# Kernel tuning notes

Hardware: AMD Instinct MI355X
Metric: run time of the kernel (lower is better)

Reference implementation:

```python
import jax, jax.numpy as jnp
import numpy as np

DIM = 256
HEADS = 8
K_RATIO = 0.25


def setup_inputs() -> dict:
    key = jax.random.key(0)
    ks = jax.random.split(key, 5)
    B, C, S = 4, DIM, 2048
    x = jax.random.normal(ks[0], (B, C, S), dtype=jnp.float32)
    # Conv1d(dim, 3*dim, 1, bias=False) weight -> (3*dim, dim)
    W_qkv = jax.random.normal(ks[1], (3 * DIM, DIM), dtype=jnp.float32) * (1.0 / np.sqrt(DIM))
    # depthwise Conv1d(3*dim, 3*dim, 3, groups=3*dim) weight -> (3*dim, 1, 3)
    W_dw = jax.random.normal(ks[2], (3 * DIM, 1, 3), dtype=jnp.float32) * (1.0 / np.sqrt(3))
    # Conv1d(dim, dim, 1, bias=False) weight -> (dim, dim)
    W_proj = jax.random.normal(ks[3], (DIM, DIM), dtype=jnp.float32) * (1.0 / np.sqrt(DIM))
    temperature = jnp.ones((HEADS, 1, 1), dtype=jnp.float32)
    return {"x": x, "W_qkv": W_qkv, "W_dw": W_dw, "W_proj": W_proj,
            "temperature": temperature}


def _l2norm(t, eps=1e-12):
    # F.normalize: x / max(||x||_2, eps)
    n = jnp.sqrt(jnp.sum(t * t, axis=-1, keepdims=True))
    return t / jnp.maximum(n, eps)


def reference(x, W_qkv, W_dw, W_proj, temperature):
    B, C, S = x.shape
    H = temperature.shape[0]
    hd = C // H
    # 1x1 conv == channel matmul
    qkv = jnp.einsum('oc,bcs->bos', W_qkv, x)  # [B, 3C, S]
    # depthwise conv, kernel 3, pad 1
    qkv = jax.lax.conv_general_dilated(
        qkv, W_dw, window_strides=(1,), padding=[(1, 1)],
        dimension_numbers=('NCH', 'OIH', 'NCH'),
        feature_group_count=3 * C)
    q, k, v = jnp.split(qkv, 3, axis=1)  # each [B, C, S]

    def to_heads(t):
        return t.reshape(B, H, hd, S).transpose(0, 1, 3, 2)  # [B, H, S, hd]

    q = _l2norm(to_heads(q))
    k = _l2norm(to_heads(k))
    v = to_heads(v)

    scores = jnp.einsum('bhsc,bhtc->bhst', q, k) * temperature  # [B,H,S,S]

    topk = max(1, min(S, int(np.ceil(K_RATIO * S))))
    vals, idx = jax.lax.top_k(scores, topk)  # [B,H,S,topk]

    # scatter top-k values into a -inf tensor along the last axis
    N = B * H * S
    sparse = jnp.full((N, S), -jnp.inf, dtype=scores.dtype)
    rows = jnp.arange(N)[:, None]
    sparse = sparse.at[rows, idx.reshape(N, topk)].set(vals.reshape(N, topk))
    sparse = jnp.clip(sparse.reshape(B, H, S, S), -10000.0, 10000.0)

    attn = jax.nn.softmax(sparse, axis=-1)  # dropout p=0.0 -> identity
    out = jnp.einsum('bhst,bhtc->bhsc', attn, v)  # [B,H,S,hd]
    out = out.transpose(0, 1, 3, 2).reshape(B, C, S)  # b (head c) s
    return jnp.einsum('oc,bcs->bos', W_proj, out)
```

## Files before the change

### kernel.cpp

```cpp
#include <hip/hip_runtime.h>
#include <math.h>

typedef __attribute__((ext_vector_type(8))) short short8;
typedef __attribute__((ext_vector_type(4))) float f32x4;
typedef __attribute__((ext_vector_type(2))) float f32x2;
typedef __attribute__((ext_vector_type(2))) unsigned int uint2v;

#define DEV __device__ __forceinline__

static constexpr int B_ = 4, C_ = 256, S_ = 2048, H_ = 8, O3_ = 768;
static constexpr int TOPK = 512;
static constexpr int QT = 16;
static constexpr int QCOLS = 512;
static constexpr int QSTR = 516;
static constexpr int QBUF = 16 * QSTR;
static constexpr int PSTH = 1024;
static constexpr int P1OFF = 2 * QBUF;
static constexpr size_t K3_LDS_BYTES = (size_t)2 * QBUF * 4;

DEV unsigned cvt_pk_bf16(float a, float b) {
  unsigned r;
  asm("v_cvt_pk_bf16_f32 %0, %1, %2" : "=v"(r) : "v"(a), "v"(b));
  return r;
}
DEV unsigned short f2bf1(float f) { return (unsigned short)(cvt_pk_bf16(f, f) & 0xFFFFu); }
DEV float bf2f(unsigned short h) { return __uint_as_float(((unsigned)h) << 16); }
DEV void hilo(float f, unsigned short& h, unsigned short& l) {
  unsigned p = cvt_pk_bf16(f, f);
  h = (unsigned short)p;
  float r = f - __uint_as_float(p << 16);
  l = (unsigned short)(cvt_pk_bf16(r, r) & 0xFFFFu);
}

__global__ void k_convw(const float* __restrict__ wqkv, const float* __restrict__ wproj,
                        unsigned short* __restrict__ wq_hi, unsigned short* __restrict__ wq_lo,
                        unsigned short* __restrict__ wproj_bf) {
  int i = blockIdx.x * 256 + threadIdx.x;
  if (i < O3_ * C_) {
    unsigned short h, l;
    hilo(wqkv[i], h, l);
    wq_hi[i] = h;
    wq_lo[i] = l;
  }
  if (i < C_ * C_) wproj_bf[i] = f2bf1(wproj[i]);
}

__global__ void k_xt(const float* __restrict__ x, unsigned short* __restrict__ xT_hi,
                     unsigned short* __restrict__ xT_lo) {
  __shared__ float t[32][33];
  int b = blockIdx.z;
  int c0 = blockIdx.y * 32, s0 = blockIdx.x * 32;
  int tx = threadIdx.x, ty = threadIdx.y;
  const float* xb = x + (size_t)b * C_ * S_;
#pragma unroll
  for (int j = 0; j < 4; ++j)
    t[ty + 8 * j][tx] = xb[(size_t)(c0 + ty + 8 * j) * S_ + s0 + tx];
  __syncthreads();
  unsigned short* hb = xT_hi + (size_t)b * S_ * C_;
  unsigned short* lb = xT_lo + (size_t)b * S_ * C_;
#pragma unroll
  for (int j = 0; j < 4; ++j) {
    unsigned short h, l;
    hilo(t[tx][ty + 8 * j], h, l);
    size_t o = (size_t)(s0 + ty + 8 * j) * C_ + c0 + tx;
    hb[o] = h;
    lb[o] = l;
  }
}

__global__ __launch_bounds__(256) void k_qkv(const unsigned short* __restrict__ w_hi,
                                             const unsigned short* __restrict__ w_lo,
                                             const unsigned short* __restrict__ x_hi,
                                             const unsigned short* __restrict__ x_lo,
                                             float* __restrict__ raw) {
  int b = blockIdx.z;
  int m0 = blockIdx.y * 64, n0 = blockIdx.x * 64;
  int tid = threadIdx.x, lane = tid & 63, wid = tid >> 6;
  int l15 = lane & 15, lh = lane >> 4;
  int wm = (wid >> 1) * 32, wn = (wid & 1) * 32;
  const unsigned short* xhb = x_hi + (size_t)b * S_ * C_;
  const unsigned short* xlb = x_lo + (size_t)b * S_ * C_;
  f32x4 acc[2][2] = {};
  int mA = m0 + wm + l15;
  int nB = n0 + wn + l15;
  for (int k0 = 0; k0 < C_; k0 += 32) {
    int kk = k0 + lh * 8;
    short8 a0h = *(const short8*)(w_hi + (size_t)mA * C_ + kk);
    short8 a1h = *(const short8*)(w_hi + (size_t)(mA + 16) * C_ + kk);
    short8 a0l = *(const short8*)(w_lo + (size_t)mA * C_ + kk);
    short8 a1l = *(const short8*)(w_lo + (size_t)(mA + 16) * C_ + kk);
    short8 b0h = *(const short8*)(xhb + (size_t)nB * C_ + kk);
    short8 b1h = *(const short8*)(xhb + (size_t)(nB + 16) * C_ + kk);
    short8 b0l = *(const short8*)(xlb + (size_t)nB * C_ + kk);
    short8 b1l = *(const short8*)(xlb + (size_t)(nB + 16) * C_ + kk);
    acc[0][0] = __builtin_amdgcn_mfma_f32_16x16x32_bf16(a0h, b0h, acc[0][0], 0, 0, 0);
    acc[0][1] = __builtin_amdgcn_mfma_f32_16x16x32_bf16(a0h, b1h, acc[0][1], 0, 0, 0);
    acc[1][0] = __builtin_amdgcn_mfma_f32_16x16x32_bf16(a1h, b0h, acc[1][0], 0, 0, 0);
    acc[1][1] = __builtin_amdgcn_mfma_f32_16x16x32_bf16(a1h, b1h, acc[1][1], 0, 0, 0);
    acc[0][0] = __builtin_amdgcn_mfma_f32_16x16x32_bf16(a0h, b0l, acc[0][0], 0, 0, 0);
    acc[0][1] = __builtin_amdgcn_mfma_f32_16x16x32_bf16(a0h, b1l, acc[0][1], 0, 0, 0);
    acc[1][0] = __builtin_amdgcn_mfma_f32_16x16x32_bf16(a1h, b0l, acc[1][0], 0, 0, 0);
    acc[1][1] = __builtin_amdgcn_mfma_f32_16x16x32_bf16(a1h, b1l, acc[1][1], 0, 0, 0);
    acc[0][0] = __builtin_amdgcn_mfma_f32_16x16x32_bf16(a0l, b0h, acc[0][0], 0, 0, 0);
    acc[0][1] = __builtin_amdgcn_mfma_f32_16x16x32_bf16(a0l, b1h, acc[0][1], 0, 0, 0);
    acc[1][0] = __builtin_amdgcn_mfma_f32_16x16x32_bf16(a1l, b0h, acc[1][0], 0, 0, 0);
    acc[1][1] = __builtin_amdgcn_mfma_f32_16x16x32_bf16(a1l, b1h, acc[1][1], 0, 0, 0);
  }
  float* rawb = raw + (size_t)b * O3_ * S_;
#pragma unroll
  for (int i = 0; i < 2; ++i)
#pragma unroll
    for (int j = 0; j < 2; ++j)
#pragma unroll
      for (int r = 0; r < 4; ++r) {
        int row = m0 + wm + i * 16 + lh * 4 + r;
        int col = n0 + wn + j * 16 + l15;
        rawb[(size_t)row * S_ + col] = acc[i][j][r];
      }
}

DEV float conv3(const float* __restrict__ rp, const float* __restrict__ w, int s) {
  float a = (s > 0) ? rp[s - 1] : 0.f;
  float b = rp[s];
  float c = (s < S_ - 1) ? rp[s + 1] : 0.f;
  return w[0] * a + w[1] * b + w[2] * c;
}

__global__ __launch_bounds__(256) void k_dwnorm(const float* __restrict__ raw,
                                                const float* __restrict__ wdw,
                                                const float* __restrict__ temp,
                                                unsigned short* __restrict__ q_hi,
                                                unsigned short* __restrict__ q_lo,
                                                unsigned short* __restrict__ k_hi,
                                                unsigned short* __restrict__ k_lo,
                                                unsigned short* __restrict__ vt) {
  int b = blockIdx.z, h = blockIdx.y;
  int tid = threadIdx.x;
  int wave = tid >> 6, lane = tid & 63;
  int dg = lane & 7;
  int sl = lane >> 3;
  int s = blockIdx.x * 32 + wave * 8 + sl;
  const float* rawb = raw + (size_t)b * O3_ * S_;
  float tph = temp[h];
  size_t bh = (size_t)(b * H_ + h);
  float qv[4], kv[4], vv[4];
  float sq = 0.f, sk = 0.f;
#pragma unroll
  for (int dd = 0; dd < 4; ++dd) {
    int d = dg * 4 + dd;
    int oq = h * 32 + d;
    float q = conv3(rawb + (size_t)oq * S_, wdw + oq * 3, s);
    qv[dd] = q; sq += q * q;
    int ok = oq + 256;
    float k = conv3(rawb + (size_t)ok * S_, wdw + ok * 3, s);
    kv[dd] = k; sk += k * k;
    int ov = oq + 512;
    vv[dd] = conv3(rawb + (size_t)ov * S_, wdw + ov * 3, s);
  }
#pragma unroll
  for (int m = 1; m < 8; m <<= 1) {
    sq += __shfl_xor(sq, m);
    sk += __shfl_xor(sk, m);
  }
  float iq = tph / fmaxf(sqrtf(sq), 1e-12f);
  float ik = 1.f / fmaxf(sqrtf(sk), 1e-12f);
  size_t base = (bh * S_ + s) * 32 + dg * 4;

  float q0 = qv[0] * iq, q1 = qv[1] * iq, q2 = qv[2] * iq, q3 = qv[3] * iq;
  unsigned qh01 = cvt_pk_bf16(q0, q1), qh23 = cvt_pk_bf16(q2, q3);
  *(uint2v*)(q_hi + base) = uint2v{qh01, qh23};
  float ql0 = q0 - __uint_as_float(qh01 << 16);
  float ql1 = q1 - __uint_as_float(qh01 & 0xFFFF0000u);
  float ql2 = q2 - __uint_as_float(qh23 << 16);
  float ql3 = q3 - __uint_as_float(qh23 & 0xFFFF0000u);
  *(uint2v*)(q_lo + base) = uint2v{cvt_pk_bf16(ql0, ql1), cvt_pk_bf16(ql2, ql3)};

  float k0 = kv[0] * ik, k1 = kv[1] * ik, k2 = kv[2] * ik, k3 = kv[3] * ik;
  unsigned kh01 = cvt_pk_bf16(k0, k1), kh23 = cvt_pk_bf16(k2, k3);
  *(uint2v*)(k_hi + base) = uint2v{kh01, kh23};
  float kl0 = k0 - __uint_as_float(kh01 << 16);
  float kl1 = k1 - __uint_as_float(kh01 & 0xFFFF0000u);
  float kl2 = k2 - __uint_as_float(kh23 << 16);
  float kl3 = k3 - __uint_as_float(kh23 & 0xFFFF0000u);
  *(uint2v*)(k_lo + base) = uint2v{cvt_pk_bf16(kl0, kl1), cvt_pk_bf16(kl2, kl3)};

#pragma unroll
  for (int dd = 0; dd < 4; ++dd) {
    int d = dg * 4 + dd;
    vt[(bh * 32 + d) * S_ + s] = f2bf1(vv[dd]);
  }
}

__global__ __launch_bounds__(1024, 8) void k_attn(const unsigned short* __restrict__ q_hi,
                                                  const unsigned short* __restrict__ q_lo,
                                                  const unsigned short* __restrict__ k_hi,
                                                  const unsigned short* __restrict__ k_lo,
                                                  const unsigned short* __restrict__ vt,
                                                  unsigned short* __restrict__ ao) {
  extern __shared__ float smem[];
  __shared__ float is_arr[QT];
  unsigned short* Pb = (unsigned short*)smem;
  float* red = smem;
  int bid = blockIdx.x;
  int tile = bid & 127;
  int bh = bid >> 7;
  int q0 = tile * QT;
  int tid = threadIdx.x, lane = tid & 63, wv = tid >> 6;
  int l15 = lane & 15, lh = lane >> 4;
  const unsigned short* vb = vt + (size_t)bh * 32 * S_;

  size_t qoff = ((size_t)bh * S_ + q0 + l15) * 32 + lh * 8;
  short8 ah = *(const short8*)(q_hi + qoff);
  short8 al = *(const short8*)(q_lo + qoff);
  size_t kbase = (size_t)bh * S_ * 32;

  float v[32];

  short8 kh0, kl0, kh1, kl1;
  {
    const unsigned short* kp = k_hi + kbase + (size_t)(wv * 32 + l15) * 32 + lh * 8;
    const unsigned short* lp = k_lo + kbase + (size_t)(wv * 32 + l15) * 32 + lh * 8;
    kh0 = *(const short8*)(kp);       kl0 = *(const short8*)(lp);
    kh1 = *(const short8*)(kp + 512); kl1 = *(const short8*)(lp + 512);
  }
#pragma unroll
  for (int qq = 0; qq < 4; ++qq) {
    float* buf = smem + (qq & 1) * QBUF;
    {
      f32x4 d0 = {}, d1 = {};
      __builtin_amdgcn_s_setprio(1);
      d0 = __builtin_amdgcn_mfma_f32_16x16x32_bf16(ah, kh0, d0, 0, 0, 0);
      d0 = __builtin_amdgcn_mfma_f32_16x16x32_bf16(ah, kl0, d0, 0, 0, 0);
      d0 = __builtin_amdgcn_mfma_f32_16x16x32_bf16(al, kh0, d0, 0, 0, 0);
      d1 = __builtin_amdgcn_mfma_f32_16x16x32_bf16(ah, kh1, d1, 0, 0, 0);
      d1 = __builtin_amdgcn_mfma_f32_16x16x32_bf16(ah, kl1, d1, 0, 0, 0);
      d1 = __builtin_amdgcn_mfma_f32_16x16x32_bf16(al, kh1, d1, 0, 0, 0);
      __builtin_amdgcn_s_setprio(0);
      int tloc = wv * 32 + l15;
#pragma unroll
      for (int r = 0; r < 4; ++r) {
        buf[(lh * 4 + r) * QSTR + tloc] = d0[r];
        buf[(lh * 4 + r) * QSTR + tloc + 16] = d1[r];
      }
      if (qq < 3) {
        int colg = (qq + 1) * QCOLS + wv * 32;
        const unsigned short* kp = k_hi + kbase + (size_t)(colg + l15) * 32 + lh * 8;
        const unsigned short* lp = k_lo + kbase + (size_t)(colg + l15) * 32 + lh * 8;
        kh0 = *(const short8*)(kp);       kl0 = *(const short8*)(lp);
        kh1 = *(const short8*)(kp + 512); kl1 = *(const short8*)(lp + 512);
      }
    }
    __syncthreads();
#pragma unroll
    for (int kk2 = 0; kk2 < 4; ++kk2) {
      f32x2 pr = *(const f32x2*)&buf[wv * QSTR + kk2 * 128 + 2 * lane];
      v[qq * 8 + kk2 * 2] = pr[0];
      v[qq * 8 + kk2 * 2 + 1] = pr[1];
    }
  }

  {
    float vmax = v[0], vmin = v[0], sum = 0.f, sqs = 0.f;
#pragma unroll
    for (int j = 0; j < 32; ++j) {
      vmax = fmaxf(vmax, v[j]); vmin = fminf(vmin, v[j]);
      sum += v[j]; sqs = fmaf(v[j], v[j], sqs);
    }
#pragma unroll
    for (int m = 1; m < 64; m <<= 1) {
      vmax = fmaxf(vmax, __shfl_xor(vmax, m));
      vmin = fminf(vmin, __shfl_xor(vmin, m));
      sum += __shfl_xor(sum, m);
      sqs += __shfl_xor(sqs, m);
    }
    float mu = sum * (1.f / 2048.f);
    float sig = sqrtf(fmaxf(sqs * (1.f / 2048.f) - mu * mu, 0.f));

    float vlo = vmin - 1e-3f, vhi = vmax;
    float flo = 1536.f, fhi = -512.f;
    int chi = 0;
    float T = vhi;
    bool exact = false;
    int lastside = 0;
    float piv = mu + 0.67449f * sig;
    if (!(piv > vlo && piv < vhi)) piv = 0.5f * (vlo + vhi);
    for (int it = 0; it < 32; ++it) {
      int c = 0;
#pragma unroll
      for (int j = 0; j < 32; ++j)
        c += (int)__popcll(__ballot(v[j] > piv));
      if (c == TOPK) { T = piv; exact = true; break; }
      if (c > TOPK) {
        if (lastside == 1) fhi *= 0.5f;
        vlo = piv; flo = (float)(c - TOPK); lastside = 1;
      } else {
        if (lastside == -1) flo *= 0.5f;
        vhi = piv; fhi = (float)(c - TOPK); chi = c; lastside = -1;
      }
      float npiv;
      if (it == 0 && sig > 1e-20f) {
        float z = (piv - mu) / sig;
        float dens = 0.398942f * __expf(-0.5f * z * z) * (2048.f / sig);
        npiv = piv + (float)(c - TOPK) / fmaxf(dens, 1e-6f);
      } else {
        npiv = vhi - fhi * (vhi - vlo) / (fhi - flo);
      }
      if (!(npiv > vlo && npiv < vhi)) npiv = 0.5f * (vlo + vhi);
      if (!(npiv > vlo && npiv < vhi)) break;
      piv = npiv;
    }
    int cntGT = exact ? TOPK : chi;
    if (!exact) T = vhi;

    unsigned selbits = 0;
#pragma unroll
    for (int j = 0; j < 32; ++j)
      if (v[j] > T) selbits |= (1u << j);
    int need = TOPK - cntGT;
    if (need > 0) {
      int base = 0;
      unsigned long long lmask = (lane == 0) ? 0ull : (~0ull >> (64 - lane));
#pragma unroll
      for (int k = 0; k < 16; ++k) {
        bool t0 = (v[2 * k] == T), t1 = (v[2 * k + 1] == T);
        unsigned long long m0 = __ballot(t0);
        unsigned long long m1 = __ballot(t1);
        int before = base + (int)__popcll(m0 & lmask) + (int)__popcll(m1 & lmask);
        int r0 = before;
        int r1 = before + (t0 ? 1 : 0);
        if (t0 && r0 < need) selbits |= (1u << (2 * k));
        if (t1 && r1 < need) selbits |= (1u << (2 * k + 1));
        base += (int)__popcll(m0) + (int)__popcll(m1);
      }
    }

    float ssum = 0.f;
#pragma unroll
    for (int j = 0; j < 32; ++j) {
      float e = ((selbits >> j) & 1u) ? __expf(v[j] - vmax) : 0.f;
      v[j] = e;
      ssum += e;
    }
#pragma unroll
    for (int m = 1; m < 64; m <<= 1) ssum += __shfl_xor(ssum, m);
    if (lane == 0) is_arr[wv] = 1.f / ssum;
  }

  f32x4 acc0 = {}, acc1 = {};
  int swz_w = (wv & 7) << 3;
  int swz_r = (l15 & 7) << 3;
#pragma unroll
  for (int kk = 0; kk < 8; ++kk) {
    int lc = (kk >> 2) * 512 + (kk & 3) * 128 + 2 * lane;
    unsigned pk = cvt_pk_bf16(v[2 * kk], v[2 * kk + 1]);
    *(unsigned*)&Pb[(wv * PSTH + lc) ^ swz_w] = pk;
  }
  __syncthreads();
  {
#pragma unroll
    for (int kk = 0; kk < 8; ++kk) {
      int lc = (kk >> 2) * 512 + (kk & 3) * 128 + 2 * lane;
      unsigned pk = cvt_pk_bf16(v[16 + 2 * kk], v[16 + 2 * kk + 1]);
      *(unsigned*)&Pb[P1OFF + ((wv * PSTH + lc) ^ swz_w)] = pk;
    }
    const unsigned short* v0p = vb + (size_t)l15 * S_ + wv * 64 + lh * 8;
    const unsigned short* v1p = v0p + 16 * S_;
#pragma unroll
    for (int kt = 0; kt < 2; ++kt) {
      int lc = wv * 64 + kt * 32 + lh * 8;
      short8 a = *(const short8*)(Pb + ((l15 * PSTH + lc) ^ swz_r));
      short8 b0 = *(const short8*)(v0p + kt * 32);
      short8 b1 = *(const short8*)(v1p + kt * 32);
      __builtin_amdgcn_s_setprio(1);
      acc0 = __builtin_amdgcn_mfma_f32_16x16x32_bf16(a, b0, acc0, 0, 0, 0);
      acc1 = __builtin_amdgcn_mfma_f32_16x16x32_bf16(a, b1, acc1, 0, 0, 0);
      __builtin_amdgcn_s_setprio(0);
    }
  }
  __syncthreads();
  {
    const unsigned short* v0p = vb + (size_t)l15 * S_ + 1024 + wv * 64 + lh * 8;
    const unsigned short* v1p = v0p + 16 * S_;
#pragma unroll
    for (int kt = 0; kt < 2; ++kt) {
      int lc = wv * 64 + kt * 32 + lh * 8;
      short8 a = *(const short8*)(Pb + P1OFF + ((l15 * PSTH + lc) ^ swz_r));
      short8 b0 = *(const short8*)(v0p + kt * 32);
      short8 b1 = *(const short8*)(v1p + kt * 32);
      __builtin_amdgcn_s_setprio(1);
      acc0 = __builtin_amdgcn_mfma_f32_16x16x32_bf16(a, b0, acc0, 0, 0, 0);
      acc1 = __builtin_amdgcn_mfma_f32_16x16x32_bf16(a, b1, acc1, 0, 0, 0);
      __builtin_amdgcn_s_setprio(0);
    }
  }
  __syncthreads();

#pragma unroll
  for (int r = 0; r < 4; ++r) {
    red[wv * 529 + (lh * 4 + r) * 33 + l15] = acc0[r];
    red[wv * 529 + (lh * 4 + r) * 33 + 16 + l15] = acc1[r];
  }
  __syncthreads();
  if (tid < 512) {
    int row = tid >> 5, d = tid & 31;
    float s = 0.f;
#pragma unroll
    for (int w = 0; w < 16; ++w) s += red[w * 529 + row * 33 + d];
    s *= is_arr[row];
    ao[((size_t)bh * S_ + q0 + row) * 32 + d] = f2bf1(s);
  }
}

__global__ __launch_bounds__(256) void k_proj(const unsigned short* __restrict__ wbf,
                                              const unsigned short* __restrict__ ao,
                                              float* __restrict__ out) {
  int b = blockIdx.z;
  int m0 = blockIdx.y * 64, n0 = blockIdx.x * 64;
  int tid = threadIdx.x, lane = tid & 63, wid = tid >> 6;
  int l15 = lane & 15, lh = lane >> 4;
  int wm = (wid >> 1) * 32, wn = (wid & 1) * 32;
  const unsigned short* aob = ao + (size_t)b * H_ * S_ * 32;
  f32x4 acc[2][2] = {};
  int mA = m0 + wm + l15;
  int nB = n0 + wn + l15;
  for (int k0 = 0; k0 < C_; k0 += 32) {
    int kk = k0 + lh * 8;
    int hh = kk >> 5;
    int dd = kk & 31;
    short8 a0 = *(const short8*)(wbf + (size_t)mA * C_ + kk);
    short8 a1 = *(const short8*)(wbf + (size_t)(mA + 16) * C_ + kk);
    short8 b0 = *(const short8*)(aob + ((size_t)hh * S_ + nB) * 32 + dd);
    short8 b1 = *(const short8*)(aob + ((size_t)hh * S_ + nB + 16) * 32 + dd);
    acc[0][0] = __builtin_amdgcn_mfma_f32_16x16x32_bf16(a0, b0, acc[0][0], 0, 0, 0);
    acc[0][1] = __builtin_amdgcn_mfma_f32_16x16x32_bf16(a0, b1, acc[0][1], 0, 0, 0);
    acc[1][0] = __builtin_amdgcn_mfma_f32_16x16x32_bf16(a1, b0, acc[1][0], 0, 0, 0);
    acc[1][1] = __builtin_amdgcn_mfma_f32_16x16x32_bf16(a1, b1, acc[1][1], 0, 0, 0);
  }
  float* ob = out + (size_t)b * C_ * S_;
#pragma unroll
  for (int i = 0; i < 2; ++i)
#pragma unroll
    for (int j = 0; j < 2; ++j)
#pragma unroll
      for (int r = 0; r < 4; ++r) {
        int row = m0 + wm + i * 16 + lh * 4 + r;
        int col = n0 + wn + j * 16 + l15;
        ob[(size_t)row * S_ + col] = acc[i][j][r];
      }
}

extern "C" void kernel_launch(void* const* d_in, const int* in_sizes, int n_in,
                              void* d_out, int out_size, void* d_ws, size_t ws_size,
                              hipStream_t stream) {
  const float* x = (const float*)d_in[0];
  const float* wqkv = (const float*)d_in[1];
  const float* wdw = (const float*)d_in[2];
  const float* wproj = (const float*)d_in[3];
  const float* temp = (const float*)d_in[4];
  float* out = (float*)d_out;

  char* ws = (char*)d_ws;
  size_t off = 0;
  auto alloc = [&](size_t bytes) -> void* {
    void* p = ws + off;
    off += (bytes + 255) & ~(size_t)255;
    return p;
  };
  unsigned short* x_hi     = (unsigned short*)alloc((size_t)B_ * S_ * C_ * 2);
  unsigned short* x_lo     = (unsigned short*)alloc((size_t)B_ * S_ * C_ * 2);
  unsigned short* wq_hi    = (unsigned short*)alloc((size_t)O3_ * C_ * 2);
  unsigned short* wq_lo    = (unsigned short*)alloc((size_t)O3_ * C_ * 2);
  unsigned short* wproj_bf = (unsigned short*)alloc((size_t)C_ * C_ * 2);
  float*          raw      = (float*)alloc((size_t)B_ * O3_ * S_ * 4);
  unsigned short* k_hi     = (unsigned short*)alloc((size_t)B_ * H_ * S_ * 32 * 2);
  unsigned short* k_lo     = (unsigned short*)alloc((size_t)B_ * H_ * S_ * 32 * 2);
  unsigned short* vt       = (unsigned short*)alloc((size_t)B_ * H_ * 32 * S_ * 2);
  unsigned short* q_hi     = x_hi;
  unsigned short* q_lo     = x_lo;
  unsigned short* ao       = (unsigned short*)raw;

  (void)hipFuncSetAttribute(reinterpret_cast<const void*>(k_attn),
                            hipFuncAttributeMaxDynamicSharedMemorySize, (int)K3_LDS_BYTES);

  k_convw<<<dim3((O3_ * C_ + 255) / 256), dim3(256), 0, stream>>>(wqkv, wproj, wq_hi, wq_lo, wproj_bf);
  k_xt<<<dim3(S_ / 32, C_ / 32, B_), dim3(32, 8), 0, stream>>>(x, x_hi, x_lo);
  k_qkv<<<dim3(S_ / 64, O3_ / 64, B_), dim3(256), 0, stream>>>(wq_hi, wq_lo, x_hi, x_lo, raw);
  k_dwnorm<<<dim3(S_ / 32, H_, B_), dim3(256), 0, stream>>>(raw, wdw, temp, q_hi, q_lo, k_hi, k_lo, vt);
  k_attn<<<dim3(B_ * H_ * (S_ / QT)), dim3(1024), K3_LDS_BYTES, stream>>>(q_hi, q_lo, k_hi, k_lo, vt, ao);
  k_proj<<<dim3(S_ / 64, C_ / 64, B_), dim3(256), 0, stream>>>(wproj_bf, ao, out);
}
```

Measured before the change: 273.1 us.

## Fuse x transpose and bf16 hi/lo split into QKV GEMM via LDS staging

Removes the separate k_xt kernel that transposed x and wrote bf16 hi/lo copies to global memory. The QKV GEMM now reads fp32 x directly, splits it into hi/lo bf16 and stages it in double-buffered padded LDS tiles for the MFMA B operand. This saves one launch and a global round trip of the transposed copy. In exchange, every m-block re-reads and re-converts x, adds block barriers, and q_hi/q_lo now need their own workspace buffers.

```diff
diff --git a/kernel.cpp b/kernel.cpp
--- a/kernel.cpp
+++ b/kernel.cpp
@@ -5,6 +5,7 @@
 typedef __attribute__((ext_vector_type(4))) float f32x4;
 typedef __attribute__((ext_vector_type(2))) float f32x2;
 typedef __attribute__((ext_vector_type(2))) unsigned int uint2v;
+typedef __attribute__((ext_vector_type(4))) unsigned int uint4v;
 
 #define DEV __device__ __forceinline__
 
@@ -17,6 +18,7 @@
 static constexpr int PSTH = 1024;
 static constexpr int P1OFF = 2 * QBUF;
 static constexpr size_t K3_LDS_BYTES = (size_t)2 * QBUF * 4;
+static constexpr int XSTR = 40;
 
 DEV unsigned cvt_pk_bf16(float a, float b) {
   unsigned r;
@@ -45,54 +47,59 @@
   if (i < C_ * C_) wproj_bf[i] = f2bf1(wproj[i]);
 }
 
-__global__ void k_xt(const float* __restrict__ x, unsigned short* __restrict__ xT_hi,
-                     unsigned short* __restrict__ xT_lo) {
-  __shared__ float t[32][33];
-  int b = blockIdx.z;
-  int c0 = blockIdx.y * 32, s0 = blockIdx.x * 32;
-  int tx = threadIdx.x, ty = threadIdx.y;
-  const float* xb = x + (size_t)b * C_ * S_;
-#pragma unroll
-  for (int j = 0; j < 4; ++j)
-    t[ty + 8 * j][tx] = xb[(size_t)(c0 + ty + 8 * j) * S_ + s0 + tx];
-  __syncthreads();
-  unsigned short* hb = xT_hi + (size_t)b * S_ * C_;
-  unsigned short* lb = xT_lo + (size_t)b * S_ * C_;
-#pragma unroll
-  for (int j = 0; j < 4; ++j) {
-    unsigned short h, l;
-    hilo(t[tx][ty + 8 * j], h, l);
-    size_t o = (size_t)(s0 + ty + 8 * j) * C_ + c0 + tx;
-    hb[o] = h;
-    lb[o] = l;
-  }
-}
-
 __global__ __launch_bounds__(256) void k_qkv(const unsigned short* __restrict__ w_hi,
                                              const unsigned short* __restrict__ w_lo,
-                                             const unsigned short* __restrict__ x_hi,
-                                             const unsigned short* __restrict__ x_lo,
+                                             const float* __restrict__ x,
                                              float* __restrict__ raw) {
+  __shared__ unsigned short xh[2][64 * XSTR];
+  __shared__ unsigned short xl[2][64 * XSTR];
   int b = blockIdx.z;
   int m0 = blockIdx.y * 64, n0 = blockIdx.x * 64;
   int tid = threadIdx.x, lane = tid & 63, wid = tid >> 6;
   int l15 = lane & 15, lh = lane >> 4;
   int wm = (wid >> 1) * 32, wn = (wid & 1) * 32;
-  const unsigned short* xhb = x_hi + (size_t)b * S_ * C_;
-  const unsigned short* xlb = x_lo + (size_t)b * S_ * C_;
+  int sl = tid & 63, cg = tid >> 6;
+  const float* xb = x + (size_t)b * C_ * S_ + n0 + sl;
+
   f32x4 acc[2][2] = {};
   int mA = m0 + wm + l15;
-  int nB = n0 + wn + l15;
-  for (int k0 = 0; k0 < C_; k0 += 32) {
-    int kk = k0 + lh * 8;
-    short8 a0h = *(const short8*)(w_hi + (size_t)mA * C_ + kk);
-    short8 a1h = *(const short8*)(w_hi + (size_t)(mA + 16) * C_ + kk);
-    short8 a0l = *(const short8*)(w_lo + (size_t)mA * C_ + kk);
-    short8 a1l = *(const short8*)(w_lo + (size_t)(mA + 16) * C_ + kk);
-    short8 b0h = *(const short8*)(xhb + (size_t)nB * C_ + kk);
-    short8 b1h = *(const short8*)(xhb + (size_t)(nB + 16) * C_ + kk);
-    short8 b0l = *(const short8*)(xlb + (size_t)nB * C_ + kk);
-    short8 b1l = *(const short8*)(xlb + (size_t)(nB + 16) * C_ + kk);
+
+  auto stage = [&](int k0, int bufi) {
+    float f[8];
+#pragma unroll
+    for (int j = 0; j < 8; ++j)
+      f[j] = xb[(size_t)(k0 + cg * 8 + j) * S_];
+    unsigned h[4], l[4];
+#pragma unroll
+    for (int j = 0; j < 4; ++j) {
+      h[j] = cvt_pk_bf16(f[2 * j], f[2 * j + 1]);
+      float r0 = f[2 * j] - __uint_as_float(h[j] << 16);
+      float r1 = f[2 * j + 1] - __uint_as_float(h[j] & 0xFFFF0000u);
+      l[j] = cvt_pk_bf16(r0, r1);
+    }
+    int o = sl * XSTR + cg * 8;
+    *(uint4v*)&xh[bufi][o] = uint4v{h[0], h[1], h[2], h[3]};
+    *(uint4v*)&xl[bufi][o] = uint4v{l[0], l[1], l[2], l[3]};
+  };
+
+  stage(0, 0);
+  for (int ks = 0; ks < 8; ++ks) {
+    __syncthreads();
+    if (ks < 7) stage((ks + 1) * 32, (ks ^ 1) & 1);
+    int kk = lh * 8;
+    int k0 = ks * 32;
+    const unsigned short* bh0 = &xh[ks & 1][(wn + l15) * XSTR + kk];
+    const unsigned short* bh1 = &xh[ks & 1][(wn + 16 + l15) * XSTR + kk];
+    const unsigned short* bl0 = &xl[ks & 1][(wn + l15) * XSTR + kk];
+    const unsigned short* bl1 = &xl[ks & 1][(wn + 16 + l15) * XSTR + kk];
+    short8 b0h = *(const short8*)bh0;
+    short8 b1h = *(const short8*)bh1;
+    short8 b0l = *(const short8*)bl0;
+    short8 b1l = *(const short8*)bl1;
+    short8 a0h = *(const short8*)(w_hi + (size_t)mA * C_ + k0 + kk);
+    short8 a1h = *(const short8*)(w_hi + (size_t)(mA + 16) * C_ + k0 + kk);
+    short8 a0l = *(const short8*)(w_lo + (size_t)mA * C_ + k0 + kk);
+    short8 a1l = *(const short8*)(w_lo + (size_t)(mA + 16) * C_ + k0 + kk);
     acc[0][0] = __builtin_amdgcn_mfma_f32_16x16x32_bf16(a0h, b0h, acc[0][0], 0, 0, 0);
     acc[0][1] = __builtin_amdgcn_mfma_f32_16x16x32_bf16(a0h, b1h, acc[0][1], 0, 0, 0);
     acc[1][0] = __builtin_amdgcn_mfma_f32_16x16x32_bf16(a1h, b0h, acc[1][0], 0, 0, 0);
@@ -466,25 +473,22 @@
     off += (bytes + 255) & ~(size_t)255;
     return p;
   };
-  unsigned short* x_hi     = (unsigned short*)alloc((size_t)B_ * S_ * C_ * 2);
-  unsigned short* x_lo     = (unsigned short*)alloc((size_t)B_ * S_ * C_ * 2);
   unsigned short* wq_hi    = (unsigned short*)alloc((size_t)O3_ * C_ * 2);
   unsigned short* wq_lo    = (unsigned short*)alloc((size_t)O3_ * C_ * 2);
   unsigned short* wproj_bf = (unsigned short*)alloc((size_t)C_ * C_ * 2);
   float*          raw      = (float*)alloc((size_t)B_ * O3_ * S_ * 4);
+  unsigned short* q_hi     = (unsigned short*)alloc((size_t)B_ * H_ * S_ * 32 * 2);
+  unsigned short* q_lo     = (unsigned short*)alloc((size_t)B_ * H_ * S_ * 32 * 2);
   unsigned short* k_hi     = (unsigned short*)alloc((size_t)B_ * H_ * S_ * 32 * 2);
   unsigned short* k_lo     = (unsigned short*)alloc((size_t)B_ * H_ * S_ * 32 * 2);
   unsigned short* vt       = (unsigned short*)alloc((size_t)B_ * H_ * 32 * S_ * 2);
-  unsigned short* q_hi     = x_hi;
-  unsigned short* q_lo     = x_lo;
   unsigned short* ao       = (unsigned short*)raw;
 
   (void)hipFuncSetAttribute(reinterpret_cast<const void*>(k_attn),
                             hipFuncAttributeMaxDynamicSharedMemorySize, (int)K3_LDS_BYTES);
 
   k_convw<<<dim3((O3_ * C_ + 255) / 256), dim3(256), 0, stream>>>(wqkv, wproj, wq_hi, wq_lo, wproj_bf);
-  k_xt<<<dim3(S_ / 32, C_ / 32, B_), dim3(32, 8), 0, stream>>>(x, x_hi, x_lo);
-  k_qkv<<<dim3(S_ / 64, O3_ / 64, B_), dim3(256), 0, stream>>>(wq_hi, wq_lo, x_hi, x_lo, raw);
+  k_qkv<<<dim3(S_ / 64, O3_ / 64, B_), dim3(256), 0, stream>>>(wq_hi, wq_lo, x, raw);
   k_dwnorm<<<dim3(S_ / 32, H_, B_), dim3(256), 0, stream>>>(raw, wdw, temp, q_hi, q_lo, k_hi, k_lo, vt);
   k_attn<<<dim3(B_ * H_ * (S_ / QT)), dim3(1024), K3_LDS_BYTES, stream>>>(q_hi, q_lo, k_hi, k_lo, vt, ao);
   k_proj<<<dim3(S_ / 64, C_ / 64, B_), dim3(256), 0, stream>>>(wproj_bf, ao, out);
```

After: 252.0 us. -7.7%, faster.
